# Optimization experiments

Hardware: AMD Instinct MI355X
Metric: run time of the kernel (lower is better)

The kernel has to match this reference:

```python
import jax, jax.numpy as jnp
import numpy as np

B, N, T, K = 128, 64, 512, 5
FS = 120.0  # sampling rate implied by rfftfreq(N, d=1/120) in FFT_for_Period


def setup_inputs() -> dict:
    key = jax.random.key(0)
    x = jax.random.normal(key, (B, N, T), dtype=jnp.float32)
    return {"x": x}


def _gather_time(S, ix):
    # S: [B, T2, N]; ix: [B, K, T] int indices along time axis -> [B, K, T, N]
    b = ix.shape[0]
    g = jnp.take_along_axis(S, ix.reshape(b, -1)[:, :, None], axis=1)
    return g.reshape(ix.shape + (S.shape[-1],))


def _fft_trend(x, k_top=K):
    # Faithful vectorization of FFT_TREND.forward: x [B, N, T] -> trends [B, N, K, T]
    xt = jnp.transpose(x, (0, 2, 1))  # [B, T, N]
    Tn = xt.shape[1]
    # FFT_for_Period: mean |rfft| over nodes, zero DC bin, top-k frequency bins
    mag = jnp.abs(jnp.fft.rfft(xt, axis=1)).mean(-1)  # [B, F]
    mag = mag.at[:, 0].set(0.0)
    _, top_idx = jax.lax.top_k(mag, k_top)  # [B, K]
    freqs = jnp.fft.rfftfreq(Tn, d=1.0 / FS).astype(jnp.float32)
    scale = jnp.floor(Tn / freqs[top_idx]).astype(jnp.int32)  # top_scale = T // top_freq, [B, K]
    # static bound: smallest nonzero freq is FS/T -> max kernel = T*T/FS
    pmax = (Tn * Tn) // int(FS)
    scale = jnp.clip(scale, 1, pmax)
    pad = (pmax - 1) // 2 + 1
    # edge-replicated extension (matches moving_avg front/end repeat padding)
    idx = jnp.clip(jnp.arange(-pad, Tn + pad), 0, Tn - 1)
    ext = xt[:, idx, :]  # [B, T + 2*pad, N]
    S = jnp.concatenate([jnp.zeros_like(ext[:, :1]), jnp.cumsum(ext, axis=1)], axis=1)
    t = jnp.arange(Tn)
    k = scale[:, :, None]                      # [B, K, 1] data-dependent kernel sizes
    p = (k - 1) // 2                           # moving_avg pad = (k-1)//2 per side
    L = Tn + 2 * p - k + 1                     # AvgPool1d output length (T odd-k, T-1 even-k)
    tc = jnp.minimum(t[None, None, :], L - 1)  # repeat-last-row fix for even kernels
    start = tc - p + pad                       # [B, K, T] window starts in ext coords
    win = _gather_time(S, start + k) - _gather_time(S, start)  # [B, K, T, N] window sums
    mean = win / k[..., None].astype(xt.dtype)                  # moving averages
    # torch: stack over K -> [K,B,T,N], permute(1,3,0,2) -> [B,N,K,T]
    return jnp.transpose(mean, (0, 3, 1, 2))


def reference(x):
    return _fft_trend(x)
```

## Files before the change

kernel.cpp:

```cpp
#include <hip/hip_runtime.h>
#include <cmath>

namespace {

constexpr int B_ = 128;
constexpr int N_ = 64;
constexpr int T_ = 512;
constexpr int K_ = 5;
constexpr int NBINS = 257;
constexpr int PMAX = 2184;
constexpr int ROWS = 4;
constexpr int FROWS = 8;
constexpr int CHUNKS = N_ / FROWS;

struct cpx { float re, im; };
__device__ __forceinline__ cpx cadd(cpx a, cpx b) { return {a.re + b.re, a.im + b.im}; }
__device__ __forceinline__ cpx csub(cpx a, cpx b) { return {a.re - b.re, a.im - b.im}; }
__device__ __forceinline__ cpx cmul(cpx a, cpx b) {
  return {a.re * b.re - a.im * b.im, a.re * b.im + a.im * b.re};
}

__device__ __forceinline__ void radix8(
    cpx z0, cpx z1, cpx z2, cpx z3, cpx z4, cpx z5, cpx z6, cpx z7,
    cpx& t0, cpx& t1, cpx& t2, cpx& t3, cpx& t4, cpx& t5, cpx& t6, cpx& t7) {
  const float c = 0.70710678118654752f;
  cpx a0 = cadd(z0, z4), a1 = csub(z0, z4);
  cpx a2 = cadd(z2, z6), a3 = csub(z2, z6);
  cpx a4 = cadd(z1, z5), a5 = csub(z1, z5);
  cpx a6 = cadd(z3, z7), a7 = csub(z3, z7);
  cpx b0 = cadd(a0, a2), b1 = csub(a0, a2);
  cpx b2 = cadd(a4, a6), b3 = csub(a4, a6);
  t0 = cadd(b0, b2);
  t4 = csub(b0, b2);
  t2 = {b1.re + b3.im, b1.im - b3.re};
  t6 = {b1.re - b3.im, b1.im + b3.re};
  cpx ua5  = {c * (a5.re + a5.im), c * (a5.im - a5.re)};
  cpx usa5 = {c * (a5.re - a5.im), c * (a5.re + a5.im)};
  cpx ua7  = {c * (a7.re + a7.im), c * (a7.im - a7.re)};
  cpx usa7 = {c * (a7.re - a7.im), c * (a7.re + a7.im)};
  cpx mia3 = {a3.im, -a3.re};
  cpx pia3 = {-a3.im, a3.re};
  t1 = cadd(cadd(a1, ua5), csub(mia3, usa7));
  t3 = cadd(csub(a1, usa5), cadd(pia3, ua7));
  t5 = cadd(csub(a1, ua5), cadd(mia3, usa7));
  t7 = cadd(cadd(a1, usa5), csub(pia3, ua7));
}

__device__ __forceinline__ void lds_fence() {
  __builtin_amdgcn_sched_barrier(0);
}

__global__ __launch_bounds__(256, 4) void fft_mag_kernel(const float* __restrict__ x,
                                                         float* __restrict__ magp) {
  const int tid = threadIdx.x;
  const int w = tid >> 6;
  const int lane = tid & 63;
  const int rowA = blockIdx.x * FROWS + 2 * w;

  __shared__ float bre[4][576];
  __shared__ float bim[4][576];

  float* br = &bre[w][0];
  float* bi = &bim[w][0];

  const float* srcA = x + ((size_t)rowA << 9);
  const float* srcB = srcA + T_;

  {
    const int j = lane;
    const cpx z0 = {srcA[j],       srcB[j]};
    const cpx z1 = {srcA[j +  64], srcB[j +  64]};
    const cpx z2 = {srcA[j + 128], srcB[j + 128]};
    const cpx z3 = {srcA[j + 192], srcB[j + 192]};
    const cpx z4 = {srcA[j + 256], srcB[j + 256]};
    const cpx z5 = {srcA[j + 320], srcB[j + 320]};
    const cpx z6 = {srcA[j + 384], srcB[j + 384]};
    const cpx z7 = {srcA[j + 448], srcB[j + 448]};
    cpx y0, y1, y2, y3, y4, y5, y6, y7;
    radix8(z0, z1, z2, z3, z4, z5, z6, z7, y0, y1, y2, y3, y4, y5, y6, y7);
    float sj, cj;
    __sincosf((float)j * 0.01227184630308513f , &sj, &cj);
    const cpx wj = {cj, -sj};
    const int p = j * 9;
    cpx tw = wj, z;
    br[p + 0] = y0.re;            bi[p + 0] = y0.im;
    z = cmul(y1, tw); br[p + 1] = z.re; bi[p + 1] = z.im; tw = cmul(tw, wj);
    z = cmul(y2, tw); br[p + 2] = z.re; bi[p + 2] = z.im; tw = cmul(tw, wj);
    z = cmul(y3, tw); br[p + 3] = z.re; bi[p + 3] = z.im; tw = cmul(tw, wj);
    z = cmul(y4, tw); br[p + 4] = z.re; bi[p + 4] = z.im; tw = cmul(tw, wj);
    z = cmul(y5, tw); br[p + 5] = z.re; bi[p + 5] = z.im; tw = cmul(tw, wj);
    z = cmul(y6, tw); br[p + 6] = z.re; bi[p + 6] = z.im; tw = cmul(tw, wj);
    z = cmul(y7, tw); br[p + 7] = z.re; bi[p + 7] = z.im;
  }
  lds_fence();

  const int r2 = lane >> 3, i2 = lane & 7;
  {
    const int p = i2 * 9 + r2;
    const cpx zz0 = {br[p +   0], bi[p +   0]};
    const cpx zz1 = {br[p +  72], bi[p +  72]};
    const cpx zz2 = {br[p + 144], bi[p + 144]};
    const cpx zz3 = {br[p + 216], bi[p + 216]};
    const cpx zz4 = {br[p + 288], bi[p + 288]};
    const cpx zz5 = {br[p + 360], bi[p + 360]};
    const cpx zz6 = {br[p + 432], bi[p + 432]};
    const cpx zz7 = {br[p + 504], bi[p + 504]};
    cpx t0, t1, t2, t3, t4, t5, t6, t7;
    radix8(zz0, zz1, zz2, zz3, zz4, zz5, zz6, zz7, t0, t1, t2, t3, t4, t5, t6, t7);
    float si, ci;
    __sincosf((float)i2 * 0.09817477042468103f , &si, &ci);
    const cpx wi = {ci, -si};
    cpx tw = wi;
    cpx y1 = cmul(t1, tw); tw = cmul(tw, wi);
    cpx y2 = cmul(t2, tw); tw = cmul(tw, wi);
    cpx y3 = cmul(t3, tw); tw = cmul(tw, wi);
    cpx y4 = cmul(t4, tw); tw = cmul(tw, wi);
    cpx y5 = cmul(t5, tw); tw = cmul(tw, wi);
    cpx y6 = cmul(t6, tw); tw = cmul(tw, wi);
    cpx y7 = cmul(t7, tw);
    lds_fence();
    const int q = r2 * 72 + i2;
    br[q +  0] = t0.re; bi[q +  0] = t0.im;
    br[q +  9] = y1.re; bi[q +  9] = y1.im;
    br[q + 18] = y2.re; bi[q + 18] = y2.im;
    br[q + 27] = y3.re; bi[q + 27] = y3.im;
    br[q + 36] = y4.re; bi[q + 36] = y4.im;
    br[q + 45] = y5.re; bi[q + 45] = y5.im;
    br[q + 54] = y6.re; bi[q + 54] = y6.im;
    br[q + 63] = y7.re; bi[q + 63] = y7.im;
  }
  lds_fence();

  {
    const int r3 = lane >> 3, c3 = lane & 7;
    const int p = r3 * 72 + c3 * 9;
    const cpx yy0 = {br[p + 0], bi[p + 0]};
    const cpx yy1 = {br[p + 1], bi[p + 1]};
    const cpx yy2 = {br[p + 2], bi[p + 2]};
    const cpx yy3 = {br[p + 3], bi[p + 3]};
    const cpx yy4 = {br[p + 4], bi[p + 4]};
    const cpx yy5 = {br[p + 5], bi[p + 5]};
    const cpx yy6 = {br[p + 6], bi[p + 6]};
    const cpx yy7 = {br[p + 7], bi[p + 7]};
    cpx X0, X1, X2, X3, X4, X5, X6, X7;
    radix8(yy0, yy1, yy2, yy3, yy4, yy5, yy6, yy7, X0, X1, X2, X3, X4, X5, X6, X7);
    lds_fence();
    const int kb0 = (c3 << 3) + r3;
    br[kb0 +   0] = X0.re; bi[kb0 +   0] = X0.im;
    br[kb0 +  64] = X1.re; bi[kb0 +  64] = X1.im;
    br[kb0 + 128] = X2.re; bi[kb0 + 128] = X2.im;
    br[kb0 + 192] = X3.re; bi[kb0 + 192] = X3.im;
    br[kb0 + 256] = X4.re; bi[kb0 + 256] = X4.im;
    br[kb0 + 320] = X5.re; bi[kb0 + 320] = X5.im;
    br[kb0 + 384] = X6.re; bi[kb0 + 384] = X6.im;
    br[kb0 + 448] = X7.re; bi[kb0 + 448] = X7.im;
  }
  lds_fence();

  {
    float m[4];
    float a0, b0, c0, d0, a1, b1, c1, d1, a2, b2, c2, d2, a3, b3, c3v, d3;
    {
      const int k0 = lane, k0m = (512 - k0) & 511;
      a0 = br[k0]; b0 = bi[k0]; c0 = br[k0m]; d0 = bi[k0m];
      const int k1 = lane + 64, k1m = 512 - k1;
      a1 = br[k1]; b1 = bi[k1]; c1 = br[k1m]; d1 = bi[k1m];
      const int k2 = lane + 128, k2m = 512 - k2;
      a2 = br[k2]; b2 = bi[k2]; c2 = br[k2m]; d2 = bi[k2m];
      const int k3 = lane + 192, k3m = 512 - k3;
      a3 = br[k3]; b3 = bi[k3]; c3v = br[k3m]; d3 = bi[k3m];
    }
    float e256r = 0.f, e256i = 0.f;
    if (lane == 0) { e256r = br[256]; e256i = bi[256]; }
    lds_fence();
    {
      const float sa = a0 + c0, dv = b0 - d0, sv = b0 + d0, du = a0 - c0;
      m[0] = 0.5f * (sqrtf(sa * sa + dv * dv) + sqrtf(sv * sv + du * du));
    }
    {
      const float sa = a1 + c1, dv = b1 - d1, sv = b1 + d1, du = a1 - c1;
      m[1] = 0.5f * (sqrtf(sa * sa + dv * dv) + sqrtf(sv * sv + du * du));
    }
    {
      const float sa = a2 + c2, dv = b2 - d2, sv = b2 + d2, du = a2 - c2;
      m[2] = 0.5f * (sqrtf(sa * sa + dv * dv) + sqrtf(sv * sv + du * du));
    }
    {
      const float sa = a3 + c3v, dv = b3 - d3, sv = b3 + d3, du = a3 - c3v;
      m[3] = 0.5f * (sqrtf(sa * sa + dv * dv) + sqrtf(sv * sv + du * du));
    }
    br[lane]       = m[0];
    br[lane + 64]  = m[1];
    br[lane + 128] = m[2];
    br[lane + 192] = m[3];
    if (lane == 0) br[256] = fabsf(e256r) + fabsf(e256i);
  }
  __syncthreads();

  for (int bin = tid; bin < NBINS; bin += 256) {
    magp[(size_t)blockIdx.x * NBINS + bin] =
        bre[0][bin] + bre[1][bin] + bre[2][bin] + bre[3][bin];
  }
}

__global__ __launch_bounds__(256) void trend_topk_kernel(const float* __restrict__ x,
                                                         const float* __restrict__ magp,
                                                         float* __restrict__ out) {
  const int tid = threadIdx.x;
  const int w = tid >> 6;
  const int lane = tid & 63;
  const int bn = blockIdx.x * ROWS + w;
  const int b = bn >> 6;

  __shared__ float m[NBINS];
  __shared__ int sc[K_];
  __shared__ float P[ROWS][T_ + 1];

  for (int i = tid; i < NBINS; i += 256) {
    float s = -1.0f;
    if (i != 0) {
      s = 0.0f;
      const float* mp = magp + (size_t)b * CHUNKS * NBINS + i;
#pragma unroll
      for (int c = 0; c < CHUNKS; ++c) s += mp[c * NBINS];
    }
    m[i] = s;
  }
  __syncthreads();

  if (w == 0) {
    float q0 = m[lane], q1 = m[lane + 64], q2 = m[lane + 128], q3 = m[lane + 192];
    float q4 = (lane == 0) ? m[256] : -1.0e30f;
    const int i0 = lane, i1 = lane + 64, i2x = lane + 128, i3 = lane + 192;
    const int i4 = (lane == 0) ? 256 : NBINS + 1;
#pragma unroll
    for (int kk = 0; kk < K_; ++kk) {
      float bv = q0; int bi = i0;
      if (q1 > bv) { bv = q1; bi = i1; }
      if (q2 > bv) { bv = q2; bi = i2x; }
      if (q3 > bv) { bv = q3; bi = i3; }
      if (q4 > bv) { bv = q4; bi = i4; }
      for (int off = 32; off > 0; off >>= 1) {
        const float ov = __shfl_down(bv, off);
        const int oi = __shfl_down(bi, off);
        if (ov > bv || (ov == bv && oi < bi)) { bv = ov; bi = oi; }
      }
      bi = __shfl(bi, 0);
      if (lane == 0) {
        int s = 32768 / (15 * bi);
        s = s < 1 ? 1 : (s > PMAX ? PMAX : s);
        sc[kk] = s;
      }
      if (bi == i0) q0 = -1.0e30f;
      else if (bi == i1) q1 = -1.0e30f;
      else if (bi == i2x) q2 = -1.0e30f;
      else if (bi == i3) q3 = -1.0e30f;
      else if (bi == i4) q4 = -1.0e30f;
    }
  }

  const float* src = x + ((size_t)bn << 9);
  const float4 v0 = *reinterpret_cast<const float4*>(src + (lane << 3));
  const float4 v1 = *reinterpret_cast<const float4*>(src + (lane << 3) + 4);

  float e0 = v0.x;
  float e1 = e0 + v0.y;
  float e2 = e1 + v0.z;
  float e3 = e2 + v0.w;
  float e4 = e3 + v1.x;
  float e5 = e4 + v1.y;
  float e6 = e5 + v1.z;
  float e7 = e6 + v1.w;

  float v = e7;
  for (int off = 1; off < 64; off <<= 1) {
    const float o = __shfl_up(v, off);
    if (lane >= off) v += o;
  }
  const float base = v - e7;

  float* Pw = P[w];
  if (lane == 0) Pw[0] = 0.0f;
  const int p0 = (lane << 3) + 1;
  Pw[p0 + 0] = base + e0;
  Pw[p0 + 1] = base + e1;
  Pw[p0 + 2] = base + e2;
  Pw[p0 + 3] = base + e3;
  Pw[p0 + 4] = base + e4;
  Pw[p0 + 5] = base + e5;
  Pw[p0 + 6] = base + e6;
  Pw[p0 + 7] = base + e7;
  __syncthreads();

  const float x0 = Pw[1];
  const float xl = Pw[T_] - Pw[T_ - 1];

  float* outbn = out + (((size_t)bn * K_) << 9);
#pragma unroll
  for (int kk = 0; kk < K_; ++kk) {
    const int k = sc[kk];
    const int p = (k - 1) >> 1;
    const int Lm1 = T_ + 2 * p - k;
    const float invk = 1.0f / (float)k;
#pragma unroll
    for (int u = 0; u < 8; ++u) {
      const int t = lane + (u << 6);
      const int tc = t < Lm1 ? t : Lm1;
      const int lo = tc - p;
      const int hi = lo + k;
      const int cl = lo < 0 ? -lo : 0;
      const int cr = hi > T_ ? hi - T_ : 0;
      const int loc = lo < 0 ? 0 : lo;
      const int hic = hi > T_ ? T_ : hi;
      const float sum = Pw[hic] - Pw[loc] + (float)cl * x0 + (float)cr * xl;
      outbn[(kk << 9) + t] = sum * invk;
    }
  }
}

}

extern "C" void kernel_launch(void* const* d_in, const int* in_sizes, int n_in,
                              void* d_out, int out_size, void* d_ws, size_t ws_size,
                              hipStream_t stream) {
  const float* x = (const float*)d_in[0];
  float* out = (float*)d_out;

  float* magp = (float*)d_ws;

  hipLaunchKernelGGL(fft_mag_kernel, dim3(B_ * N_ / FROWS), dim3(256), 0, stream, x, magp);
  hipLaunchKernelGGL(trend_topk_kernel, dim3(B_ * N_ / ROWS), dim3(256), 0, stream, x, magp, out);
}
```

Before: 32.89 us.

## Pair mirror FFT bins via shuffles and fold partial-magnitude reduction into top-k warp

In the FFT kernel, the final radix-8 outputs are paired with their conjugate-mirror bins through cross-lane shuffles. The two-real-signal magnitudes are computed in registers and only the magnitudes go to LDS, which removes a full complex LDS write/read round trip and a fence. In the trend kernel, warp 0 sums the per-chunk partial magnitudes straight into its registers instead of going through a shared array and a block barrier. The x row loads are moved earlier to overlap with that work, and outputs use nontemporal stores. The shuffle partner mapping is subtle and must exactly reproduce the earlier bin pairing.

```diff
diff --git a/kernel.cpp b/kernel.cpp
--- a/kernel.cpp
+++ b/kernel.cpp
@@ -144,56 +144,42 @@
     const cpx yy7 = {br[p + 7], bi[p + 7]};
     cpx X0, X1, X2, X3, X4, X5, X6, X7;
     radix8(yy0, yy1, yy2, yy3, yy4, yy5, yy6, yy7, X0, X1, X2, X3, X4, X5, X6, X7);
+
+    const int partner = lane == 0 ? 0 : (lane < 8 ? 8 - lane : 71 - lane);
+    float m0r = __shfl(X7.re, partner), m0i = __shfl(X7.im, partner);
+    float m1r = __shfl(X6.re, partner), m1i = __shfl(X6.im, partner);
+    float m2r = __shfl(X5.re, partner), m2i = __shfl(X5.im, partner);
+    float m3r = __shfl(X4.re, partner), m3i = __shfl(X4.im, partner);
+    if (lane == 0) {
+      m0r = X0.re; m0i = X0.im;
+      m1r = X7.re; m1i = X7.im;
+      m2r = X6.re; m2i = X6.im;
+      m3r = X5.re; m3i = X5.im;
+    }
+    float g0, g1, g2, g3;
+    {
+      const float sa = X0.re + m0r, dv = X0.im - m0i, sv = X0.im + m0i, du = X0.re - m0r;
+      g0 = 0.5f * (sqrtf(sa * sa + dv * dv) + sqrtf(sv * sv + du * du));
+    }
+    {
+      const float sa = X1.re + m1r, dv = X1.im - m1i, sv = X1.im + m1i, du = X1.re - m1r;
+      g1 = 0.5f * (sqrtf(sa * sa + dv * dv) + sqrtf(sv * sv + du * du));
+    }
+    {
+      const float sa = X2.re + m2r, dv = X2.im - m2i, sv = X2.im + m2i, du = X2.re - m2r;
+      g2 = 0.5f * (sqrtf(sa * sa + dv * dv) + sqrtf(sv * sv + du * du));
+    }
+    {
+      const float sa = X3.re + m3r, dv = X3.im - m3i, sv = X3.im + m3i, du = X3.re - m3r;
+      g3 = 0.5f * (sqrtf(sa * sa + dv * dv) + sqrtf(sv * sv + du * du));
+    }
     lds_fence();
-    const int kb0 = (c3 << 3) + r3;
-    br[kb0 +   0] = X0.re; bi[kb0 +   0] = X0.im;
-    br[kb0 +  64] = X1.re; bi[kb0 +  64] = X1.im;
-    br[kb0 + 128] = X2.re; bi[kb0 + 128] = X2.im;
-    br[kb0 + 192] = X3.re; bi[kb0 + 192] = X3.im;
-    br[kb0 + 256] = X4.re; bi[kb0 + 256] = X4.im;
-    br[kb0 + 320] = X5.re; bi[kb0 + 320] = X5.im;
-    br[kb0 + 384] = X6.re; bi[kb0 + 384] = X6.im;
-    br[kb0 + 448] = X7.re; bi[kb0 + 448] = X7.im;
-  }
-  lds_fence();
-
-  {
-    float m[4];
-    float a0, b0, c0, d0, a1, b1, c1, d1, a2, b2, c2, d2, a3, b3, c3v, d3;
-    {
-      const int k0 = lane, k0m = (512 - k0) & 511;
-      a0 = br[k0]; b0 = bi[k0]; c0 = br[k0m]; d0 = bi[k0m];
-      const int k1 = lane + 64, k1m = 512 - k1;
-      a1 = br[k1]; b1 = bi[k1]; c1 = br[k1m]; d1 = bi[k1m];
-      const int k2 = lane + 128, k2m = 512 - k2;
-      a2 = br[k2]; b2 = bi[k2]; c2 = br[k2m]; d2 = bi[k2m];
-      const int k3 = lane + 192, k3m = 512 - k3;
-      a3 = br[k3]; b3 = bi[k3]; c3v = br[k3m]; d3 = bi[k3m];
-    }
-    float e256r = 0.f, e256i = 0.f;
-    if (lane == 0) { e256r = br[256]; e256i = bi[256]; }
-    lds_fence();
-    {
-      const float sa = a0 + c0, dv = b0 - d0, sv = b0 + d0, du = a0 - c0;
-      m[0] = 0.5f * (sqrtf(sa * sa + dv * dv) + sqrtf(sv * sv + du * du));
-    }
-    {
-      const float sa = a1 + c1, dv = b1 - d1, sv = b1 + d1, du = a1 - c1;
-      m[1] = 0.5f * (sqrtf(sa * sa + dv * dv) + sqrtf(sv * sv + du * du));
-    }
-    {
-      const float sa = a2 + c2, dv = b2 - d2, sv = b2 + d2, du = a2 - c2;
-      m[2] = 0.5f * (sqrtf(sa * sa + dv * dv) + sqrtf(sv * sv + du * du));
-    }
-    {
-      const float sa = a3 + c3v, dv = b3 - d3, sv = b3 + d3, du = a3 - c3v;
-      m[3] = 0.5f * (sqrtf(sa * sa + dv * dv) + sqrtf(sv * sv + du * du));
-    }
-    br[lane]       = m[0];
-    br[lane + 64]  = m[1];
-    br[lane + 128] = m[2];
-    br[lane + 192] = m[3];
-    if (lane == 0) br[256] = fabsf(e256r) + fabsf(e256i);
+    const int kb = ((lane & 7) << 3) | (lane >> 3);
+    br[kb +   0] = g0;
+    br[kb +  64] = g1;
+    br[kb + 128] = g2;
+    br[kb + 192] = g3;
+    if (lane == 0) br[256] = fabsf(X4.re) + fabsf(X4.im);
   }
   __syncthreads();
 
@@ -212,25 +198,27 @@
   const int bn = blockIdx.x * ROWS + w;
   const int b = bn >> 6;
 
-  __shared__ float m[NBINS];
   __shared__ int sc[K_];
   __shared__ float P[ROWS][T_ + 1];
 
-  for (int i = tid; i < NBINS; i += 256) {
-    float s = -1.0f;
-    if (i != 0) {
-      s = 0.0f;
-      const float* mp = magp + (size_t)b * CHUNKS * NBINS + i;
+  const float* src = x + ((size_t)bn << 9);
+  const float4 v0 = *reinterpret_cast<const float4*>(src + (lane << 3));
+  const float4 v1 = *reinterpret_cast<const float4*>(src + (lane << 3) + 4);
+
+  if (w == 0) {
+    const float* mb = magp + (size_t)b * CHUNKS * NBINS;
+    float q0 = 0.f, q1 = 0.f, q2 = 0.f, q3 = 0.f, q4 = 0.f;
 #pragma unroll
-      for (int c = 0; c < CHUNKS; ++c) s += mp[c * NBINS];
-    }
-    m[i] = s;
-  }
-  __syncthreads();
-
-  if (w == 0) {
-    float q0 = m[lane], q1 = m[lane + 64], q2 = m[lane + 128], q3 = m[lane + 192];
-    float q4 = (lane == 0) ? m[256] : -1.0e30f;
+    for (int c = 0; c < CHUNKS; ++c) {
+      const float* mc = mb + c * NBINS;
+      q0 += mc[lane];
+      q1 += mc[lane + 64];
+      q2 += mc[lane + 128];
+      q3 += mc[lane + 192];
+      if (lane == 0) q4 += mc[256];
+    }
+    if (lane == 0) q0 = -1.0f;
+    if (lane != 0) q4 = -1.0e30f;
     const int i0 = lane, i1 = lane + 64, i2x = lane + 128, i3 = lane + 192;
     const int i4 = (lane == 0) ? 256 : NBINS + 1;
 #pragma unroll
@@ -259,10 +247,6 @@
     }
   }
 
-  const float* src = x + ((size_t)bn << 9);
-  const float4 v0 = *reinterpret_cast<const float4*>(src + (lane << 3));
-  const float4 v1 = *reinterpret_cast<const float4*>(src + (lane << 3) + 4);
-
   float e0 = v0.x;
   float e1 = e0 + v0.y;
   float e2 = e1 + v0.z;
@@ -313,7 +297,7 @@
       const int loc = lo < 0 ? 0 : lo;
       const int hic = hi > T_ ? T_ : hi;
       const float sum = Pw[hic] - Pw[loc] + (float)cl * x0 + (float)cr * xl;
-      outbn[(kk << 9) + t] = sum * invk;
+      __builtin_nontemporal_store(sum * invk, &outbn[(kk << 9) + t]);
     }
   }
 }
```

New measurement: 35.63 us. +8.4%, slower.
